# Kernel optimization log

Hardware: AMD Instinct MI355X
Metric: run time of the kernel (lower is better)

## Reference

```python
import jax, jax.numpy as jnp
from jax import lax
import numpy as np

B, C, H, W = 8, 256, 192, 192
ATT_K = 11
BN_EPS = 1e-5


def _dwconv(x, w, pad, stride=1):
    # x: NCHW, w: (C,1,kh,kw) depthwise
    return lax.conv_general_dilated(
        x, w, window_strides=(stride, stride), padding=pad,
        feature_group_count=x.shape[1],
        dimension_numbers=('NCHW', 'OIHW', 'NCHW'))


def _max_pool_3x3(x):
    return lax.reduce_window(x, -jnp.inf, lax.max,
                             (1, 1, 3, 3), (1, 1, 1, 1), 'SAME')


def _blur_pool(x, stride=3):
    # antialiased_cnns.BlurPool, filt_size=4: reflect pad [1,2,1,2], binomial 4x4, depthwise, stride 3
    c = x.shape[1]
    a = jnp.array([1., 3., 3., 1.], dtype=x.dtype)
    filt = (a[:, None] * a[None, :])
    filt = filt / jnp.sum(filt)
    w = jnp.tile(filt[None, None], (c, 1, 1, 1))  # (C,1,4,4)
    xp = jnp.pad(x, ((0, 0), (0, 0), (1, 2), (1, 2)), mode='reflect')
    return _dwconv(xp, w, 'VALID', stride=stride)


def _h_transform(x):
    b, c, h, w = x.shape
    x = jnp.pad(x, ((0, 0), (0, 0), (0, 0), (0, w)))
    x = x.reshape(b, c, -1)[..., :-w]
    return x.reshape(b, c, h, 2 * w - 1)


def _inv_h_transform(x):
    b, c, h, _ = x.shape  # last dim = 2h-1 (requires square)
    x = x.reshape(b, c, -1)
    x = jnp.pad(x, ((0, 0), (0, 0), (0, h)))
    x = x.reshape(b, c, h, 2 * h)
    return x[..., :h]


def _v_transform(x):
    return jnp.transpose(_h_transform(jnp.transpose(x, (0, 1, 3, 2))), (0, 1, 3, 2))


def _inv_v_transform(x):
    return jnp.transpose(_inv_h_transform(jnp.transpose(x, (0, 1, 3, 2))), (0, 1, 3, 2))


def setup_inputs() -> dict:
    key = jax.random.key(0)
    ks = jax.random.split(key, 5)
    pad = ATT_K // 2
    return {
        'x': jax.random.normal(ks[0], (B, C, H, W), dtype=jnp.float32),
        'w_h1': jax.random.normal(ks[1], (C, 1, ATT_K, 3), dtype=jnp.float32) * 0.1,
        'w_v1': jax.random.normal(ks[2], (C, 1, 3, ATT_K), dtype=jnp.float32) * 0.1,
        'w_h2': jax.random.normal(ks[3], (C, 1, ATT_K, 3), dtype=jnp.float32) * 0.1,
        'w_v2': jax.random.normal(ks[4], (C, 1, 3, ATT_K), dtype=jnp.float32) * 0.1,
        'bn_gamma': jnp.ones((C,), dtype=jnp.float32),
        'bn_beta': jnp.zeros((C,), dtype=jnp.float32),
        'bn_mean': jnp.zeros((C,), dtype=jnp.float32),
        'bn_var': jnp.ones((C,), dtype=jnp.float32),
    }


def reference(x, w_h1, w_v1, w_h2, w_v2, bn_gamma, bn_beta, bn_mean, bn_var):
    pad = ATT_K // 2
    b, c, h, w = x.shape

    x_tem = _max_pool_3x3(x)
    x_tem = _blur_pool(x_tem, stride=3)  # (B,C,64,64)

    x_h1 = _dwconv(x_tem, w_h1, ((pad, pad), (1, 1)))
    x_w1 = _dwconv(x_tem, w_v1, ((1, 1), (pad, pad)))

    # h == w (192 == 192): diagonal branch active
    x_h2 = _inv_h_transform(_dwconv(_h_transform(x_tem), w_h2, ((pad, pad), (1, 1))))
    x_w2 = _inv_v_transform(_dwconv(_v_transform(x_tem), w_v2, ((1, 1), (pad, pad))))

    s = x_h1 + x_w1 + x_h2 + x_w2
    # inference BatchNorm2d
    inv = bn_gamma / jnp.sqrt(bn_var + BN_EPS)
    att = (s - bn_mean[None, :, None, None]) * inv[None, :, None, None] + bn_beta[None, :, None, None]

    gate = jax.nn.sigmoid(att)
    # nearest interpolate to (h, w): idx = floor(i * in/out)
    ah, aw = gate.shape[2], gate.shape[3]
    idx_h = (jnp.arange(h) * ah) // h
    idx_w = (jnp.arange(w) * aw) // w
    gate_up = gate[:, :, idx_h][:, :, :, idx_w]

    return x[:, :c] * gate_up
```

## Files before the change

kernel.cpp:

```cpp
#include <hip/hip_runtime.h>
#include <hip/hip_fp16.h>
#include <math.h>

#define BN_EPS 1e-5f

typedef _Float16 h2v __attribute__((ext_vector_type(2)));

__device__ __forceinline__ float max3f(float a, float b, float c) {
    return fmaxf(fmaxf(a, b), c);
}
__device__ __forceinline__ float fdot2u(uint32_t a, uint32_t b, float c) {
    union U { uint32_t u; h2v h; } ua, ub;
    ua.u = a; ub.u = b;
    return __builtin_amdgcn_fdot2(ua.h, ub.h, c, false);
}
__device__ __forceinline__ uint32_t pack2(float a, float b) {
    union U { uint32_t u; h2v h; } x;
    x.h.x = (_Float16)a; x.h.y = (_Float16)b; return x.u;
}

__global__ __launch_bounds__(512, 8)
void mra_fused(const float* __restrict__ x,
               const float* __restrict__ wh1,
               const float* __restrict__ wv1,
               const float* __restrict__ wh2,
               const float* __restrict__ wv2,
               const float* __restrict__ bng,
               const float* __restrict__ bnb,
               const float* __restrict__ bnm,
               const float* __restrict__ bnv,
               float* __restrict__ out)
{
    __shared__ __align__(16) __half sxp_h[76][84];
    __shared__ __align__(16) __half gate_h[64][72];
    __shared__ __align__(16) uint32_t wtab[13][12];

    const int plane = blockIdx.x;
    const int c     = plane & 255;
    const int tid   = threadIdx.x;
    const int lane  = tid & 63;
    const int w     = tid >> 6;
    const float* __restrict__ xp = x   + (size_t)plane * 36864;
    float* __restrict__       op = out + (size_t)plane * 36864;

    const float* __restrict__ wh1p = wh1 + c * 33;
    const float* __restrict__ wv1p = wv1 + c * 33;
    const float* __restrict__ wh2p = wh2 + c * 33;
    const float* __restrict__ wv2p = wv2 + c * 33;

    {
        int* z = (int*)&sxp_h[0][0];
        const int nInt = (76 * 84 * 2) / 4;
        #pragma unroll
        for (int i = 0; i < 7; ++i) {
            const int idx = tid + (i << 9);
            if (idx < nInt) z[idx] = 0;
        }
    }
    if (tid < 13) {
        const int e = tid - 6;
        uint32_t* wr = wtab[tid];
        #pragma unroll
        for (int s = 0; s < 12; ++s) wr[s] = 0;
        if (e >= -5 && e <= 5) {
            const float* a1 = wh1p + (e + 5) * 3;
            wr[0] = pack2(a1[0], a1[1]); wr[1] = pack2(a1[2], 0.f);
            const float* a2 = wh2p + (e + 5) * 3;
            wr[2] = pack2(a2[0], a2[1]); wr[3] = pack2(a2[2], 0.f);
        }
        if (e >= -4 && e <= 4) {
            wr[4] = pack2(wv2p[4 - e], wv2p[16 - e]);
            wr[5] = pack2(wv2p[28 - e], 0.f);
        } else if (e == 5)  wr[4] = pack2(wv2p[11], wv2p[23]);
        else if (e == -5)   wr[4] = pack2(wv2p[9],  wv2p[21]);
        else if (e == 6)    wr[4] = pack2(wv2p[22], 0.f);
        else                wr[4] = pack2(wv2p[10], 0.f);
        if (e >= -1 && e <= 1) {
            const float* a3 = wv1p + (e + 1) * 11;
            wr[6]  = pack2(a3[0], a3[1]); wr[7]  = pack2(a3[2], a3[3]);
            wr[8]  = pack2(a3[4], a3[5]); wr[9]  = pack2(a3[6], a3[7]);
            wr[10] = pack2(a3[8], a3[9]); wr[11] = pack2(a3[10], 0.f);
        }
    }
    __syncthreads();

    {
        const int P0  = w << 3;
        const int r0  = 3 * P0 - 2;
        const int col = 3 * lane;

        float c0r[4], c1r[4], c2r[4];
        auto issue = [&](int k, int s) {
            int r = r0 + k;
            r = r < 0 ? 0 : (r > 191 ? 191 : r);
            const float* rp = xp + r * 192 + col;
            c0r[s] = rp[0]; c1r[s] = rp[1]; c2r[s] = rp[2];
        };
        issue(0, 0); issue(1, 1); issue(2, 2); issue(3, 3);

        float h[3][4];
        float hb[3];
        float hbp = 0.f;

        #pragma unroll
        for (int k = 0; k < 27; ++k) {
            const int s = k & 3;
            const float c0 = c0r[s], c1 = c1r[s], c2 = c2r[s];
            if (k + 4 < 27) issue(k + 4, s);

            float xm2 = __shfl_up(c1, 1);
            float xm1 = __shfl_up(c2, 1);
            float xp3 = __shfl_down(c0, 1);
            if (lane == 0)  xm1 = c0;
            if (lane == 63) xp3 = c2;

            const float hm_m1 = max3f(xm2, xm1, c0);
            const float hm_0  = max3f(xm1, c0,  c1);
            const float hm_1  = max3f(c0,  c1,  c2);
            const float hm_2  = max3f(c1,  c2,  xp3);

            float* hk = h[k % 3];
            hk[0] = (lane == 0) ? hm_1 : hm_m1;
            hk[1] = hm_0; hk[2] = hm_1; hk[3] = hm_2;

            if (k >= 2) {
                const float* a = h[(k - 2) % 3];
                const float* b = h[(k - 1) % 3];
                const float* d = h[k % 3];
                const float e4 =
                      0.125f * max3f(a[0], b[0], d[0])
                    + 0.375f * max3f(a[1], b[1], d[1])
                    + 0.375f * max3f(a[2], b[2], d[2])
                    + 0.125f * max3f(a[3], b[3], d[3]);
                if (k == 2) {
                    hbp = e4;
                } else {
                    hb[k % 3] = e4;
                    if (k % 3 == 2) {
                        const int i = (k - 5) / 3;
                        float a_out;
                        if (i == 0 && w == 0)
                            a_out = 0.375f * hb[0] + 0.5f * hb[1] + 0.125f * hb[2];
                        else
                            a_out = 0.125f * hbp + 0.375f * hb[0]
                                  + 0.375f * hb[1] + 0.125f * hb[2];
                        hbp = hb[2];
                        sxp_h[(w << 3) + i + 6][lane + 8] = __float2half(a_out);
                    }
                }
            }
        }
    }
    __syncthreads();

    const int p  = tid >> 3;
    const int q0 = (tid & 7) << 3;
    float acc[8];
    #pragma unroll
    for (int i = 0; i < 8; ++i) acc[i] = 0.0f;

    #pragma unroll
    for (int e = -6; e <= 6; ++e) {
        const uint2* drow = (const uint2*)&sxp_h[p + e + 6][q0];
        uint32_t du[12], su[11];
        #pragma unroll
        for (int u2 = 0; u2 < 6; ++u2) {
            const uint2 t = drow[u2];
            du[2 * u2] = t.x; du[2 * u2 + 1] = t.y;
        }
        #pragma unroll
        for (int u = 0; u < 11; ++u)
            su[u] = __builtin_amdgcn_alignbit(du[u + 1], du[u], 16);

        const uint2* wrow = (const uint2*)&wtab[e + 6][0];
        const uint2 wa = wrow[0], wb = wrow[1], wc = wrow[2];

        auto RUN3 = [&](float a, int j0, uint32_t pA, uint32_t pB) -> float {
            const int u = j0 >> 1;
            if (j0 & 1) { a = fdot2u(su[u], pA, a); a = fdot2u(su[u + 1], pB, a); }
            else        { a = fdot2u(du[u], pA, a); a = fdot2u(du[u + 1], pB, a); }
            return a;
        };
        auto RUN1 = [&](float a, int j0, uint32_t pA) -> float {
            const int u = j0 >> 1;
            return (j0 & 1) ? fdot2u(su[u], pA, a) : fdot2u(du[u], pA, a);
        };

        if (e >= -5 && e <= 5) {
            #pragma unroll
            for (int i = 0; i < 8; ++i) {
                acc[i] = RUN3(acc[i], i + 7, wa.x, wa.y);
                acc[i] = RUN3(acc[i], i + 7 - e, wb.x, wb.y);
            }
        }
        if (e >= -4 && e <= 4) {
            #pragma unroll
            for (int i = 0; i < 8; ++i) acc[i] = RUN3(acc[i], i + 7 - e, wc.x, wc.y);
        } else if (e == 5) {
            #pragma unroll
            for (int i = 0; i < 8; ++i) acc[i] = RUN1(acc[i], i + 3, wc.x);
        } else if (e == -5) {
            #pragma unroll
            for (int i = 0; i < 8; ++i) acc[i] = RUN1(acc[i], i + 12, wc.x);
        } else if (e == 6) {
            #pragma unroll
            for (int i = 0; i < 8; ++i) acc[i] = RUN1(acc[i], i + 3, wc.x);
        } else {
            #pragma unroll
            for (int i = 0; i < 8; ++i) acc[i] = RUN1(acc[i], i + 13, wc.x);
        }
        if (e >= -1 && e <= 1) {
            const uint2 wd = wrow[3], we_ = wrow[4], wf_ = wrow[5];
            const uint32_t wp[6] = {wd.x, wd.y, we_.x, we_.y, wf_.x, wf_.y};
            #pragma unroll
            for (int i = 0; i < 8; ++i) {
                const int j0 = i + 3;
                const int u  = j0 >> 1;
                float a = acc[i];
                #pragma unroll
                for (int kk = 0; kk < 6; ++kk)
                    a = (j0 & 1) ? fdot2u(su[u + kk], wp[kk], a)
                                 : fdot2u(du[u + kk], wp[kk], a);
                acc[i] = a;
            }
        }
    }

    const float inv = bng[c] * rsqrtf(bnv[c] + BN_EPS);
    const float mu  = bnm[c];
    const float bt  = bnb[c];
    #pragma unroll
    for (int i = 0; i < 4; ++i) {
        const float a0 = (acc[2 * i]     - mu) * inv + bt;
        const float a1 = (acc[2 * i + 1] - mu) * inv + bt;
        const float g0 = 1.0f / (1.0f + __expf(-a0));
        const float g1 = 1.0f / (1.0f + __expf(-a1));
        *(__half2*)(&gate_h[p][q0 + 2 * i]) = __floats2half2_rn(g0, g1);
    }
    __builtin_amdgcn_wave_barrier();

    const float4* __restrict__ x4 = (const float4*)xp + w * 1152;
    float4* __restrict__       o4 = (float4*)op       + w * 1152;
    int rlj[3], gcj[3], rrj[3];
    #pragma unroll
    for (int j = 0; j < 3; ++j) {
        const int idx0 = lane + (j << 6);
        const int rw   = idx0 / 48;
        const int c4   = idx0 - rw * 48;
        rlj[j] = rw;
        const int jb = c4 << 2;
        gcj[j] = jb / 3;
        rrj[j] = jb - 3 * gcj[j];
    }
    #pragma unroll
    for (int u = 0; u < 6; ++u) {
        #pragma unroll
        for (int j = 0; j < 3; ++j) {
            const int row_l = rlj[j] + (u << 2);
            const int idx   = lane + ((u * 3 + j) << 6);
            const int gr    = (w << 3) + row_l / 3;
            const float g0 = __half2float(gate_h[gr][gcj[j]]);
            const float g1 = __half2float(gate_h[gr][gcj[j] + 1]);
            const float4 xv = x4[idx];
            float4 ov;
            const float s1 = (rrj[j] == 2) ? g1 : g0;
            const float s2 = (rrj[j] >= 1) ? g1 : g0;
            ov.x = xv.x * g0;
            ov.y = xv.y * s1;
            ov.z = xv.z * s2;
            ov.w = xv.w * g1;
            o4[idx] = ov;
        }
    }
}

extern "C" void kernel_launch(void* const* d_in, const int* in_sizes, int n_in,
                              void* d_out, int out_size, void* d_ws, size_t ws_size,
                              hipStream_t stream) {
    const float* x   = (const float*)d_in[0];
    const float* wh1 = (const float*)d_in[1];
    const float* wv1 = (const float*)d_in[2];
    const float* wh2 = (const float*)d_in[3];
    const float* wv2 = (const float*)d_in[4];
    const float* g   = (const float*)d_in[5];
    const float* b   = (const float*)d_in[6];
    const float* m   = (const float*)d_in[7];
    const float* v   = (const float*)d_in[8];

    mra_fused<<<dim3(8 * 256), dim3(512), 0, stream>>>(
        x, wh1, wv1, wh2, wv2, g, b, m, v, (float*)d_out);
}
```

Measured before the change: 156.4 us.

## Process two planes per block and overlap gating stores with next plane's convolution

Each block now handles two adjacent channel planes. The output gating pass for the first plane is interleaved with the depthwise-conv compute of the second plane, so global memory traffic overlaps with fdot2 math. The grid is halved and shared memory grows, with duplicated gate and weight tables. The cost is lower parallelism, more LDS use per block and higher register pressure from carrying the accumulators alongside the streaming loads.

```diff
diff --git a/kernel.cpp b/kernel.cpp
--- a/kernel.cpp
+++ b/kernel.cpp
@@ -32,21 +32,19 @@
                float* __restrict__ out)
 {
     __shared__ __align__(16) __half sxp_h[76][84];
-    __shared__ __align__(16) __half gate_h[64][72];
-    __shared__ __align__(16) uint32_t wtab[13][12];
-
-    const int plane = blockIdx.x;
-    const int c     = plane & 255;
-    const int tid   = threadIdx.x;
-    const int lane  = tid & 63;
-    const int w     = tid >> 6;
-    const float* __restrict__ xp = x   + (size_t)plane * 36864;
-    float* __restrict__       op = out + (size_t)plane * 36864;
-
-    const float* __restrict__ wh1p = wh1 + c * 33;
-    const float* __restrict__ wv1p = wv1 + c * 33;
-    const float* __restrict__ wh2p = wh2 + c * 33;
-    const float* __restrict__ wv2p = wv2 + c * 33;
+    __shared__ __align__(16) __half gate_h[2][64][72];
+    __shared__ __align__(16) uint32_t wtab[2][13][12];
+
+    const int bid  = blockIdx.x;
+    const int p0g  = bid << 1;
+    const int c0   = p0g & 255;
+    const int tid  = threadIdx.x;
+    const int lane = tid & 63;
+    const int w    = tid >> 6;
+    const float* __restrict__ xp0 = x   + (size_t)p0g * 36864;
+    const float* __restrict__ xp1 = xp0 + 36864;
+    float* __restrict__       op0 = out + (size_t)p0g * 36864;
+    float* __restrict__       op1 = op0 + 36864;
 
     {
         int* z = (int*)&sxp_h[0][0];
@@ -57,9 +55,16 @@
             if (idx < nInt) z[idx] = 0;
         }
     }
-    if (tid < 13) {
-        const int e = tid - 6;
-        uint32_t* wr = wtab[tid];
+    if (tid < 26) {
+        const int tabi = tid / 13;
+        const int er   = tid - 13 * tabi;
+        const int e    = er - 6;
+        const int cc   = c0 + tabi;
+        const float* wh1p = wh1 + cc * 33;
+        const float* wv1p = wv1 + cc * 33;
+        const float* wh2p = wh2 + cc * 33;
+        const float* wv2p = wv2 + cc * 33;
+        uint32_t* wr = wtab[tabi][er];
         #pragma unroll
         for (int s = 0; s < 12; ++s) wr[s] = 0;
         if (e >= -5 && e <= 5) {
@@ -84,7 +89,7 @@
     }
     __syncthreads();
 
-    {
+    auto phaseA = [&](const float* __restrict__ xp) {
         const int P0  = w << 3;
         const int r0  = 3 * P0 - 2;
         const int col = 3 * lane;
@@ -105,19 +110,19 @@
         #pragma unroll
         for (int k = 0; k < 27; ++k) {
             const int s = k & 3;
-            const float c0 = c0r[s], c1 = c1r[s], c2 = c2r[s];
+            const float cc0 = c0r[s], cc1 = c1r[s], cc2 = c2r[s];
             if (k + 4 < 27) issue(k + 4, s);
 
-            float xm2 = __shfl_up(c1, 1);
-            float xm1 = __shfl_up(c2, 1);
-            float xp3 = __shfl_down(c0, 1);
-            if (lane == 0)  xm1 = c0;
-            if (lane == 63) xp3 = c2;
-
-            const float hm_m1 = max3f(xm2, xm1, c0);
-            const float hm_0  = max3f(xm1, c0,  c1);
-            const float hm_1  = max3f(c0,  c1,  c2);
-            const float hm_2  = max3f(c1,  c2,  xp3);
+            float xm2 = __shfl_up(cc1, 1);
+            float xm1 = __shfl_up(cc2, 1);
+            float xp3 = __shfl_down(cc0, 1);
+            if (lane == 0)  xm1 = cc0;
+            if (lane == 63) xp3 = cc2;
+
+            const float hm_m1 = max3f(xm2, xm1, cc0);
+            const float hm_0  = max3f(xm1, cc0, cc1);
+            const float hm_1  = max3f(cc0, cc1, cc2);
+            const float hm_2  = max3f(cc1, cc2, xp3);
 
             float* hk = h[k % 3];
             hk[0] = (lane == 0) ? hm_1 : hm_m1;
@@ -150,17 +155,12 @@
                 }
             }
         }
-    }
-    __syncthreads();
+    };
 
     const int p  = tid >> 3;
     const int q0 = (tid & 7) << 3;
-    float acc[8];
-    #pragma unroll
-    for (int i = 0; i < 8; ++i) acc[i] = 0.0f;
-
-    #pragma unroll
-    for (int e = -6; e <= 6; ++e) {
+
+    auto bIter = [&](int e, const uint32_t* __restrict__ wrowu, float* acc) {
         const uint2* drow = (const uint2*)&sxp_h[p + e + 6][q0];
         uint32_t du[12], su[11];
         #pragma unroll
@@ -172,7 +172,7 @@
         for (int u = 0; u < 11; ++u)
             su[u] = __builtin_amdgcn_alignbit(du[u + 1], du[u], 16);
 
-        const uint2* wrow = (const uint2*)&wtab[e + 6][0];
+        const uint2* wrow = (const uint2*)wrowu;
         const uint2 wa = wrow[0], wb = wrow[1], wc = wrow[2];
 
         auto RUN3 = [&](float a, int j0, uint32_t pA, uint32_t pB) -> float {
@@ -224,23 +224,22 @@
                 acc[i] = a;
             }
         }
-    }
-
-    const float inv = bng[c] * rsqrtf(bnv[c] + BN_EPS);
-    const float mu  = bnm[c];
-    const float bt  = bnb[c];
-    #pragma unroll
-    for (int i = 0; i < 4; ++i) {
-        const float a0 = (acc[2 * i]     - mu) * inv + bt;
-        const float a1 = (acc[2 * i + 1] - mu) * inv + bt;
-        const float g0 = 1.0f / (1.0f + __expf(-a0));
-        const float g1 = 1.0f / (1.0f + __expf(-a1));
-        *(__half2*)(&gate_h[p][q0 + 2 * i]) = __floats2half2_rn(g0, g1);
-    }
-    __builtin_amdgcn_wave_barrier();
-
-    const float4* __restrict__ x4 = (const float4*)xp + w * 1152;
-    float4* __restrict__       o4 = (float4*)op       + w * 1152;
+    };
+
+    auto bnStore = [&](const float* acc, int cc, __half (*gate)[72]) {
+        const float inv = bng[cc] * rsqrtf(bnv[cc] + BN_EPS);
+        const float mu  = bnm[cc];
+        const float bt  = bnb[cc];
+        #pragma unroll
+        for (int i = 0; i < 4; ++i) {
+            const float a0 = (acc[2 * i]     - mu) * inv + bt;
+            const float a1 = (acc[2 * i + 1] - mu) * inv + bt;
+            const float g0 = 1.0f / (1.0f + __expf(-a0));
+            const float g1 = 1.0f / (1.0f + __expf(-a1));
+            *(__half2*)(&gate[p][q0 + 2 * i]) = __floats2half2_rn(g0, g1);
+        }
+    };
+
     int rlj[3], gcj[3], rrj[3];
     #pragma unroll
     for (int j = 0; j < 3; ++j) {
@@ -252,25 +251,67 @@
         gcj[j] = jb / 3;
         rrj[j] = jb - 3 * gcj[j];
     }
-    #pragma unroll
-    for (int u = 0; u < 6; ++u) {
-        #pragma unroll
-        for (int j = 0; j < 3; ++j) {
-            const int row_l = rlj[j] + (u << 2);
-            const int idx   = lane + ((u * 3 + j) << 6);
-            const int gr    = (w << 3) + row_l / 3;
-            const float g0 = __half2float(gate_h[gr][gcj[j]]);
-            const float g1 = __half2float(gate_h[gr][gcj[j] + 1]);
-            const float4 xv = x4[idx];
-            float4 ov;
-            const float s1 = (rrj[j] == 2) ? g1 : g0;
-            const float s2 = (rrj[j] >= 1) ? g1 : g0;
-            ov.x = xv.x * g0;
-            ov.y = xv.y * s1;
-            ov.z = xv.z * s2;
-            ov.w = xv.w * g1;
-            o4[idx] = ov;
-        }
+    auto cChunk = [&](int ch, const float4* __restrict__ x4,
+                      float4* __restrict__ o4, __half (*gate)[72]) {
+        const int j     = ch % 3;
+        const int u     = ch / 3;
+        const int row_l = rlj[j] + (u << 2);
+        const int idx   = w * 1152 + lane + (ch << 6);
+        const int gr    = (w << 3) + row_l / 3;
+        const float g0 = __half2float(gate[gr][gcj[j]]);
+        const float g1 = __half2float(gate[gr][gcj[j] + 1]);
+        const float4 xv = x4[idx];
+        float4 ov;
+        const float s1 = (rrj[j] == 2) ? g1 : g0;
+        const float s2 = (rrj[j] >= 1) ? g1 : g0;
+        ov.x = xv.x * g0;
+        ov.y = xv.y * s1;
+        ov.z = xv.z * s2;
+        ov.w = xv.w * g1;
+        o4[idx] = ov;
+    };
+
+    phaseA(xp0);
+    __syncthreads();
+
+    {
+        float acc[8];
+        #pragma unroll
+        for (int i = 0; i < 8; ++i) acc[i] = 0.f;
+        #pragma unroll
+        for (int e = -6; e <= 6; ++e) bIter(e, wtab[0][e + 6], acc);
+        bnStore(acc, c0, gate_h[0]);
+    }
+    __syncthreads();
+
+    phaseA(xp1);
+    __syncthreads();
+
+    {
+        float acc[8];
+        #pragma unroll
+        for (int i = 0; i < 8; ++i) acc[i] = 0.f;
+        const float4* x40 = (const float4*)xp0;
+        float4*       o40 = (float4*)op0;
+        #pragma unroll
+        for (int e = -6; e <= 6; ++e) {
+            bIter(e, wtab[1][e + 6], acc);
+            if (e <= -2) {
+                cChunk(2 * (e + 6),     x40, o40, gate_h[0]);
+                cChunk(2 * (e + 6) + 1, x40, o40, gate_h[0]);
+            } else {
+                cChunk(10 + (e + 1),    x40, o40, gate_h[0]);
+            }
+        }
+        bnStore(acc, c0 + 1, gate_h[1]);
+    }
+    __builtin_amdgcn_wave_barrier();
+
+    {
+        const float4* x41 = (const float4*)xp1;
+        float4*       o41 = (float4*)op1;
+        #pragma unroll
+        for (int ch = 0; ch < 18; ++ch) cChunk(ch, x41, o41, gate_h[1]);
     }
 }
 
@@ -287,6 +328,6 @@
     const float* m   = (const float*)d_in[7];
     const float* v   = (const float*)d_in[8];
 
-    mra_fused<<<dim3(8 * 256), dim3(512), 0, stream>>>(
+    mra_fused<<<dim3(4 * 256), dim3(512), 0, stream>>>(
         x, wh1, wv1, wh2, wv2, g, b, m, v, (float*)d_out);
 }
```

Result: slower. 473.8 us (+202.9%).
